# Performance work log

Hardware: AMD Instinct MI355X
Metric: run time of the kernel (lower is better)

The kernel has to match this reference:

```python
import jax, jax.numpy as jnp
import numpy as np

E = 128
H = 4
D = E // H  # 32


def setup_inputs() -> dict:
    key = jax.random.key(0)
    ks = jax.random.split(key, 5)
    b, n = 4, 4096
    x = jax.random.normal(ks[0], (b, n, E), dtype=jnp.float32)
    # Linear weights stored as [in, out] (i.e. torch weight transposed)
    W_qkv = jax.random.normal(ks[1], (E, 3 * E), dtype=jnp.float32) * (1.0 / np.sqrt(E))
    b_qkv = jax.random.normal(ks[2], (3 * E,), dtype=jnp.float32) * 0.01
    W_proj = jax.random.normal(ks[3], (E, E), dtype=jnp.float32) * (1.0 / np.sqrt(E))
    b_proj = jax.random.normal(ks[4], (E,), dtype=jnp.float32) * 0.01
    return {"x": x, "W_qkv": W_qkv, "b_qkv": b_qkv, "W_proj": W_proj, "b_proj": b_proj}


def reference(x, W_qkv, b_qkv, W_proj, b_proj):
    b, n, e = x.shape
    # qkv projection; last dim layout is (h d qkv) with qkv innermost,
    # matching rearrange('b n (h d qkv) -> qkv b h n d')
    qkv = (x @ W_qkv + b_qkv).reshape(b, n, H, D, 3)
    qkv = jnp.transpose(qkv, (4, 0, 2, 1, 3))  # [3, b, h, n, d]
    q, k, v = qkv[0], qkv[1], qkv[2]
    # NOTE: original scales by sqrt(e) (=sqrt(128)), not sqrt(d). Faithful.
    scale = 1.0 / np.float32(np.sqrt(e))
    scores = jnp.einsum('bhnd,bhmd->bhnm', q, k) * scale  # [b,h,n,n]
    att = jax.nn.softmax(scores, axis=-1)
    # dropout is identity in eval mode (reference baseline)
    out = jnp.einsum('bhnm,bhmd->bhnd', att, v)  # [b,h,n,d]
    out = jnp.transpose(out, (0, 2, 1, 3)).reshape(b, n, e)  # b n (h d)
    return out @ W_proj + b_proj
```

## Files before the change

### kernel.cpp

```cpp
#include <hip/hip_runtime.h>
#include <stdint.h>

#define N_SEQ 4096
#define MFMA16 __builtin_amdgcn_mfma_f32_16x16x32_bf16

typedef float f32x4 __attribute__((ext_vector_type(4)));
typedef float f32x2 __attribute__((ext_vector_type(2)));
typedef unsigned short u16x8 __attribute__((ext_vector_type(8)));
typedef unsigned short u16x4 __attribute__((ext_vector_type(4)));
typedef unsigned int u32x2 __attribute__((ext_vector_type(2)));
typedef __bf16 bf16x8 __attribute__((ext_vector_type(8)));

static __device__ __forceinline__ float bf2f(unsigned short u) {
    unsigned v = ((unsigned)u) << 16;
    return __builtin_bit_cast(float, v);
}

__global__ __launch_bounds__(256) void wrepack_kernel(
    const float* __restrict__ Wq, unsigned short* __restrict__ WqF)
{
    int idx = blockIdx.x * 256 + threadIdx.x;
    int i = idx & 7, l = (idx >> 3) & 63, fr = idx >> 9;
    int ct = fr >> 2, ks = fr & 3;
    int k = ks * 32 + (l >> 4) * 8 + i;
    int col = ct * 16 + (l & 15);
    WqF[idx] = __builtin_bit_cast(unsigned short, (__bf16)Wq[k * 384 + col]);
}

__global__ __launch_bounds__(256) void qkv_kernel(
    const float* __restrict__ x, const unsigned short* __restrict__ WqF,
    const float* __restrict__ bq, unsigned short* __restrict__ Qo,
    unsigned short* __restrict__ KFo, unsigned short* __restrict__ VFo)
{
    const int tid = threadIdx.x, lane = tid & 63, w = tid >> 6;
    const int g = lane >> 4, lo = lane & 15;
    const long r0 = (long)blockIdx.x * 32;
    const float SL = (float)(0.08838834764831845 * 1.4426950408889634);
    const f32x4 zf = {0.f, 0.f, 0.f, 0.f};

    bf16x8 xf[2][4];
    #pragma unroll
    for (int rt = 0; rt < 2; ++rt) {
        const float* xr = x + (r0 + rt * 16 + lo) * 128 + g * 8;
        #pragma unroll
        for (int ks = 0; ks < 4; ++ks) {
            f32x4 a = *(const f32x4*)&xr[ks * 32];
            f32x4 b = *(const f32x4*)&xr[ks * 32 + 4];
            bf16x8 f;
            f[0] = (__bf16)a[0]; f[1] = (__bf16)a[1]; f[2] = (__bf16)a[2]; f[3] = (__bf16)a[3];
            f[4] = (__bf16)b[0]; f[5] = (__bf16)b[1]; f[6] = (__bf16)b[2]; f[7] = (__bf16)b[3];
            xf[rt][ks] = f;
        }
    }
    f32x4 acc[2][6];
    #pragma unroll
    for (int rt = 0; rt < 2; ++rt)
        #pragma unroll
        for (int c = 0; c < 6; ++c) acc[rt][c] = zf;

    const u16x8* wp = (const u16x8*)WqF + (size_t)(w * 24) * 64 + lane;
    #pragma unroll
    for (int c = 0; c < 6; ++c)
        #pragma unroll
        for (int ks = 0; ks < 4; ++ks) {
            bf16x8 wf = __builtin_bit_cast(bf16x8, wp[(c * 4 + ks) * 64]);
            acc[0][c] = MFMA16(xf[0][ks], wf, acc[0][c], 0, 0, 0);
            acc[1][c] = MFMA16(xf[1][ks], wf, acc[1][c], 0, 0, 0);
        }

    const int bb = (int)(r0 >> 12), nn0 = (int)(r0 & 4095);
    const int bh = bb * 4 + w;
    const int t = nn0 >> 6, kvb = nn0 & 63;
    const int kk = kvb >> 5;
    #pragma unroll
    for (int c = 0; c < 6; ++c) {
        int col = (w * 6 + c) * 16 + lo;
        int rem = col - w * 96;
        int d = rem / 3, s = rem % 3;
        float bias = bq[col];
        #pragma unroll
        for (int rt = 0; rt < 2; ++rt) {
            float scale = (s == 0) ? SL : 1.0f;
            unsigned short bits[4];
            #pragma unroll
            for (int j = 0; j < 4; ++j)
                bits[j] = __builtin_bit_cast(unsigned short,
                              (__bf16)((acc[rt][c][j] + bias) * scale));
            if (s == 0) {
                long base = ((long)bh * 4096 + nn0 + rt * 16 + 4 * g) * 32 + d;
                #pragma unroll
                for (int j = 0; j < 4; ++j) Qo[base + (long)j * 32] = bits[j];
            } else if (s == 1) {
                int ct_k = (kvb >> 4) + rt;
                long base = (long)((bh * 64 + t) * 4 + ct_k) * 512
                          + ((d >> 3) * 16 + 4 * g) * 8 + (d & 7);
                #pragma unroll
                for (int j = 0; j < 4; ++j) KFo[base + j * 8] = bits[j];
            } else {
                int lg = rt * 2 + (g >> 1);
                long base = (long)(((bh * 64 + t) * 2 + kk) * 2 + (d >> 4)) * 512
                          + (lg * 16 + (d & 15)) * 8 + ((4 * g) & 7);
                u16x4 pk = {bits[0], bits[1], bits[2], bits[3]};
                *(u16x4*)&VFo[base] = pk;
            }
        }
    }
}

__global__ __launch_bounds__(256, 4) void attn_kernel(
    const unsigned short* __restrict__ Q, const unsigned short* __restrict__ KF,
    const unsigned short* __restrict__ VF, unsigned short* __restrict__ AO)
{
    __shared__ __align__(16) unsigned short P_lds[4][2][2048];

    const int tid = threadIdx.x, lane = tid & 63, w = tid >> 6;
    const int g = lane >> 4, lo = lane & 15;
    const int wq = w & 1, wh = w >> 1;

    const int bid = blockIdx.x;
    const int vid = (bid & 7) * 128 + (bid >> 3);
    const int qi = vid & 63, bh = vid >> 6;
    const int q0 = qi * 64 + wq * 32;

    bf16x8 qf[2];
    #pragma unroll
    for (int rt = 0; rt < 2; ++rt) {
        const unsigned short* p = Q + ((long)bh * 4096 + q0 + rt * 16 + lo) * 32 + g * 8;
        qf[rt] = __builtin_bit_cast(bf16x8, *(const u16x8*)p);
    }
    bf16x8 onesf;
    {
        u16x8 ou = {0x3F80,0x3F80,0x3F80,0x3F80,0x3F80,0x3F80,0x3F80,0x3F80};
        onesf = __builtin_bit_cast(bf16x8, ou);
    }
    const f32x4 zf = {0.f, 0.f, 0.f, 0.f};
    f32x4 o_[2][2] = {{zf, zf}, {zf, zf}};
    f32x4 ls[2]    = {zf, zf};

    int woff[2][4], roff[2][2];
    #pragma unroll
    for (int qt = 0; qt < 2; ++qt) {
        int q = lo + 16 * qt;
        #pragma unroll
        for (int ct = 0; ct < 4; ++ct) {
            int kvb = 16 * ct + 4 * g;
            woff[qt][ct] = q * 64 + (((kvb >> 3) ^ (q & 7)) * 8) + ((kvb >> 2) & 1) * 4;
        }
    }
    #pragma unroll
    for (int rt = 0; rt < 2; ++rt) {
        int q = lo + 16 * rt;
        #pragma unroll
        for (int kk = 0; kk < 2; ++kk)
            roff[rt][kk] = q * 64 + ((((4 * kk) + g) ^ (q & 7)) * 8);
    }
    unsigned short* B0 = &P_lds[w][0][0];
    unsigned short* B1 = &P_lds[w][1][0];

    const u16x8* kp = (const u16x8*)KF + ((long)bh * 64 + wh * 32) * 256 + lane;
    const u16x8* vp = (const u16x8*)VF + ((long)bh * 64 + wh * 32) * 256 + lane;

    u16x8 K0[4], K1[4], V0[4], V1[4];
    #pragma unroll
    for (int i = 0; i < 4; ++i) K0[i] = kp[i * 64];
    kp += 256;

#define BODY(KC, KN, VP, VC, BW, BR, DOPV) do {                                \
    _Pragma("unroll")                                                          \
    for (int i = 0; i < 4; ++i) KN[i] = kp[i * 64];                            \
    kp += 256;                                                                 \
    _Pragma("unroll")                                                          \
    for (int i = 0; i < 4; ++i) VC[i] = vp[i * 64];                            \
    vp += 256;                                                                 \
    u16x8 pa_[2][2];                                                           \
    if (DOPV) {                                                                \
        _Pragma("unroll")                                                      \
        for (int kk = 0; kk < 2; ++kk)                                         \
            _Pragma("unroll")                                                  \
            for (int rt = 0; rt < 2; ++rt)                                     \
                pa_[kk][rt] = *(const u16x8*)&BR[roff[rt][kk]];                \
    }                                                                          \
    f32x4 s_[2][4];                                                            \
    _Pragma("unroll")                                                          \
    for (int ct = 0; ct < 4; ++ct) {                                           \
        bf16x8 kfr = __builtin_bit_cast(bf16x8, KC[ct]);                       \
        s_[0][ct] = MFMA16(kfr, qf[0], zf, 0, 0, 0);                           \
        s_[1][ct] = MFMA16(kfr, qf[1], zf, 0, 0, 0);                           \
    }                                                                          \
    if (DOPV) {                                                                \
        _Pragma("unroll")                                                      \
        for (int kk = 0; kk < 2; ++kk)                                         \
            _Pragma("unroll")                                                  \
            for (int rt = 0; rt < 2; ++rt) {                                   \
                bf16x8 paf = __builtin_bit_cast(bf16x8, pa_[kk][rt]);          \
                ls[rt] = MFMA16(paf, onesf, ls[rt], 0, 0, 0);                  \
                o_[rt][0] = MFMA16(paf, __builtin_bit_cast(bf16x8, VP[kk*2+0]),\
                                   o_[rt][0], 0, 0, 0);                        \
                o_[rt][1] = MFMA16(paf, __builtin_bit_cast(bf16x8, VP[kk*2+1]),\
                                   o_[rt][1], 0, 0, 0);                        \
            }                                                                  \
    }                                                                          \
    _Pragma("unroll")                                                          \
    for (int qt = 0; qt < 2; ++qt)                                             \
        _Pragma("unroll")                                                      \
        for (int ct = 0; ct < 4; ++ct) {                                       \
            unsigned b0 = __builtin_bit_cast(unsigned,                         \
                __builtin_amdgcn_exp2f(s_[qt][ct][0])) + 0x8000u;              \
            unsigned b1 = __builtin_bit_cast(unsigned,                         \
                __builtin_amdgcn_exp2f(s_[qt][ct][1])) + 0x8000u;              \
            unsigned b2 = __builtin_bit_cast(unsigned,                         \
                __builtin_amdgcn_exp2f(s_[qt][ct][2])) + 0x8000u;              \
            unsigned b3 = __builtin_bit_cast(unsigned,                         \
                __builtin_amdgcn_exp2f(s_[qt][ct][3])) + 0x8000u;              \
            u32x2 wv_;                                                         \
            wv_[0] = __builtin_amdgcn_perm(b1, b0, 0x07060302u);               \
            wv_[1] = __builtin_amdgcn_perm(b3, b2, 0x07060302u);               \
            *(u16x4*)&BW[woff[qt][ct]] = __builtin_bit_cast(u16x4, wv_);       \
        }                                                                      \
    __builtin_amdgcn_sched_barrier(0);                                         \
} while (0)

    BODY(K0, K1, V1, V0, B0, B1, 0);
    #pragma unroll 1
    for (int t = 1; t < 31; t += 2) {
        BODY(K1, K0, V0, V1, B1, B0, 1);
        BODY(K0, K1, V1, V0, B0, B1, 1);
    }
    BODY(K1, K0, V0, V1, B1, B0, 1);
#undef BODY

    #pragma unroll
    for (int kk = 0; kk < 2; ++kk)
        #pragma unroll
        for (int rt = 0; rt < 2; ++rt) {
            bf16x8 paf = __builtin_bit_cast(bf16x8, *(const u16x8*)&B1[roff[rt][kk]]);
            ls[rt] = MFMA16(paf, onesf, ls[rt], 0, 0, 0);
            o_[rt][0] = MFMA16(paf, __builtin_bit_cast(bf16x8, V1[kk*2+0]), o_[rt][0], 0, 0, 0);
            o_[rt][1] = MFMA16(paf, __builtin_bit_cast(bf16x8, V1[kk*2+1]), o_[rt][1], 0, 0, 0);
        }

    __syncthreads();
    float* sc = (float*)&P_lds[0][0][0];
    float* myp = sc + (wq * 64 + lane) * 24;
    if (wh == 1) {
        #pragma unroll
        for (int rt = 0; rt < 2; ++rt)
            #pragma unroll
            for (int dt = 0; dt < 2; ++dt)
                *(f32x4*)&myp[(rt * 2 + dt) * 4] = o_[rt][dt];
        *(f32x4*)&myp[16] = ls[0];
        *(f32x4*)&myp[20] = ls[1];
    }
    __syncthreads();
    if (wh == 0) {
        #pragma unroll
        for (int rt = 0; rt < 2; ++rt) {
            #pragma unroll
            for (int dt = 0; dt < 2; ++dt)
                o_[rt][dt] += *(const f32x4*)&myp[(rt * 2 + dt) * 4];
            ls[rt] += *(const f32x4*)&myp[16 + rt * 4];
        }
        const int bb = bh >> 2, h = bh & 3;
        #pragma unroll
        for (int rt = 0; rt < 2; ++rt)
            #pragma unroll
            for (int j = 0; j < 4; ++j) {
                float rl = __builtin_amdgcn_rcpf(ls[rt][j]);
                int row = q0 + rt * 16 + 4 * g + j;
                #pragma unroll
                for (int dt = 0; dt < 2; ++dt) {
                    int e = h * 32 + lo + 16 * dt;
                    float val = o_[rt][dt][j] * rl;
                    AO[((long)bb * N_SEQ + row) * 128 + e] =
                        __builtin_bit_cast(unsigned short, (__bf16)val);
                }
            }
    }
}

__global__ __launch_bounds__(256) void proj_kernel(
    const unsigned short* __restrict__ ain, const float* __restrict__ Wp,
    const float* __restrict__ bp, float* __restrict__ out)
{
    __shared__ __align__(16) float xT[128][36];
    const int tid = threadIdx.x;
    const long r0 = (long)blockIdx.x * 32;
    #pragma unroll
    for (int i = 0; i < 2; ++i) {
        int idx = i * 256 + tid;
        int row = idx >> 4, kc = (idx & 15) * 8;
        u16x8 v = *(const u16x8*)&ain[(r0 + row) * 128 + kc];
        #pragma unroll
        for (int e = 0; e < 8; ++e) xT[kc + e][row] = bf2f(v[e]);
    }
    __syncthreads();
    const int r8 = (tid >> 6) * 8;
    const int c  = tid & 63;
    float acc0[8], acc1[8];
    #pragma unroll
    for (int r = 0; r < 8; ++r) { acc0[r] = 0.f; acc1[r] = 0.f; }
    for (int k = 0; k < 128; ++k) {
        f32x4 a0 = *(const f32x4*)&xT[k][r8];
        f32x4 a1 = *(const f32x4*)&xT[k][r8 + 4];
        float xr[8] = {a0[0],a0[1],a0[2],a0[3],a1[0],a1[1],a1[2],a1[3]};
        float w0 = Wp[k * 128 + c];
        float w1 = Wp[k * 128 + c + 64];
        #pragma unroll
        for (int r = 0; r < 8; ++r) {
            acc0[r] = fmaf(xr[r], w0, acc0[r]);
            acc1[r] = fmaf(xr[r], w1, acc1[r]);
        }
    }
    float b0 = bp[c], b1 = bp[c + 64];
    #pragma unroll
    for (int r = 0; r < 8; ++r) {
        long n = r0 + r8 + r;
        out[n * 128 + c]      = acc0[r] + b0;
        out[n * 128 + c + 64] = acc1[r] + b1;
    }
}

extern "C" void kernel_launch(void* const* d_in, const int* in_sizes, int n_in,
                              void* d_out, int out_size, void* d_ws, size_t ws_size,
                              hipStream_t stream)
{
    const float* x  = (const float*)d_in[0];
    const float* Wq = (const float*)d_in[1];
    const float* bq = (const float*)d_in[2];
    const float* Wp = (const float*)d_in[3];
    const float* bp = (const float*)d_in[4];
    float* out = (float*)d_out;

    unsigned short* Qw   = (unsigned short*)d_ws;
    unsigned short* KFw  = Qw  + (size_t)16 * 4096 * 32;
    unsigned short* VFw  = KFw + (size_t)16 * 4096 * 32;
    unsigned short* AOw  = VFw + (size_t)16 * 4096 * 32;
    unsigned short* WqFw = AOw + (size_t)16 * 4096 * 32;

    wrepack_kernel<<<192, 256, 0, stream>>>(Wq, WqFw);
    qkv_kernel<<<512, 256, 0, stream>>>(x, WqFw, bq, Qw, KFw, VFw);
    attn_kernel<<<1024, 256, 0, stream>>>(Qw, KFw, VFw, AOw);
    proj_kernel<<<512, 256, 0, stream>>>(AOw, Wp, bp, out);
}
```

Measured before the change: 93.22 us.

## Split attention KV range four ways per block with 32-query blocks

The attention kernel now gives each block 32 query rows and splits the KV sequence across all four waves, each taking a quarter. Before, each block held 64 queries split over two query waves and two KV halves. The grid doubles to 2048 blocks and the per-wave P staging drops from two LDS buffers to one, freeing shared memory for a three-way partial-sum combine with a padded stride of 25 floats. This aims at more parallelism and shorter per-wave loops. In exchange, each K/V tile is read for half as many queries, the cross-wave reduction is larger, and the odd stride makes the 16-byte LDS accesses unaligned.

```diff
diff --git a/kernel.cpp b/kernel.cpp
--- a/kernel.cpp
+++ b/kernel.cpp
@@ -111,16 +111,15 @@
     const unsigned short* __restrict__ Q, const unsigned short* __restrict__ KF,
     const unsigned short* __restrict__ VF, unsigned short* __restrict__ AO)
 {
-    __shared__ __align__(16) unsigned short P_lds[4][2][2048];
+    __shared__ __align__(16) unsigned char smem[19456];
 
     const int tid = threadIdx.x, lane = tid & 63, w = tid >> 6;
     const int g = lane >> 4, lo = lane & 15;
-    const int wq = w & 1, wh = w >> 1;
 
     const int bid = blockIdx.x;
-    const int vid = (bid & 7) * 128 + (bid >> 3);
-    const int qi = vid & 63, bh = vid >> 6;
-    const int q0 = qi * 64 + wq * 32;
+    const int vid = (bid & 7) * 256 + (bid >> 3);
+    const int qi = vid & 127, bh = vid >> 7;
+    const int q0 = qi * 32;
 
     bf16x8 qf[2];
     #pragma unroll
@@ -154,18 +153,17 @@
         for (int kk = 0; kk < 2; ++kk)
             roff[rt][kk] = q * 64 + ((((4 * kk) + g) ^ (q & 7)) * 8);
     }
-    unsigned short* B0 = &P_lds[w][0][0];
-    unsigned short* B1 = &P_lds[w][1][0];
-
-    const u16x8* kp = (const u16x8*)KF + ((long)bh * 64 + wh * 32) * 256 + lane;
-    const u16x8* vp = (const u16x8*)VF + ((long)bh * 64 + wh * 32) * 256 + lane;
+    unsigned short* B = (unsigned short*)(smem + w * 4096);
+
+    const u16x8* kp = (const u16x8*)KF + ((long)bh * 64 + w * 16) * 256 + lane;
+    const u16x8* vp = (const u16x8*)VF + ((long)bh * 64 + w * 16) * 256 + lane;
 
     u16x8 K0[4], K1[4], V0[4], V1[4];
     #pragma unroll
     for (int i = 0; i < 4; ++i) K0[i] = kp[i * 64];
     kp += 256;
 
-#define BODY(KC, KN, VP, VC, BW, BR, DOPV) do {                                \
+#define BODY(KC, KN, VP, VC, DOPV) do {                                        \
     _Pragma("unroll")                                                          \
     for (int i = 0; i < 4; ++i) KN[i] = kp[i * 64];                            \
     kp += 256;                                                                 \
@@ -178,7 +176,7 @@
         for (int kk = 0; kk < 2; ++kk)                                         \
             _Pragma("unroll")                                                  \
             for (int rt = 0; rt < 2; ++rt)                                     \
-                pa_[kk][rt] = *(const u16x8*)&BR[roff[rt][kk]];                \
+                pa_[kk][rt] = *(const u16x8*)&B[roff[rt][kk]];                 \
     }                                                                          \
     f32x4 s_[2][4];                                                            \
     _Pragma("unroll")                                                          \
@@ -215,34 +213,34 @@
             u32x2 wv_;                                                         \
             wv_[0] = __builtin_amdgcn_perm(b1, b0, 0x07060302u);               \
             wv_[1] = __builtin_amdgcn_perm(b3, b2, 0x07060302u);               \
-            *(u16x4*)&BW[woff[qt][ct]] = __builtin_bit_cast(u16x4, wv_);       \
+            *(u16x4*)&B[woff[qt][ct]] = __builtin_bit_cast(u16x4, wv_);        \
         }                                                                      \
     __builtin_amdgcn_sched_barrier(0);                                         \
 } while (0)
 
-    BODY(K0, K1, V1, V0, B0, B1, 0);
+    BODY(K0, K1, V1, V0, 0);
     #pragma unroll 1
-    for (int t = 1; t < 31; t += 2) {
-        BODY(K1, K0, V0, V1, B1, B0, 1);
-        BODY(K0, K1, V1, V0, B0, B1, 1);
-    }
-    BODY(K1, K0, V0, V1, B1, B0, 1);
+    for (int t = 1; t < 15; t += 2) {
+        BODY(K1, K0, V0, V1, 1);
+        BODY(K0, K1, V1, V0, 1);
+    }
+    BODY(K1, K0, V0, V1, 1);
 #undef BODY
 
     #pragma unroll
     for (int kk = 0; kk < 2; ++kk)
         #pragma unroll
         for (int rt = 0; rt < 2; ++rt) {
-            bf16x8 paf = __builtin_bit_cast(bf16x8, *(const u16x8*)&B1[roff[rt][kk]]);
+            bf16x8 paf = __builtin_bit_cast(bf16x8, *(const u16x8*)&B[roff[rt][kk]]);
             ls[rt] = MFMA16(paf, onesf, ls[rt], 0, 0, 0);
             o_[rt][0] = MFMA16(paf, __builtin_bit_cast(bf16x8, V1[kk*2+0]), o_[rt][0], 0, 0, 0);
             o_[rt][1] = MFMA16(paf, __builtin_bit_cast(bf16x8, V1[kk*2+1]), o_[rt][1], 0, 0, 0);
         }
 
     __syncthreads();
-    float* sc = (float*)&P_lds[0][0][0];
-    float* myp = sc + (wq * 64 + lane) * 24;
-    if (wh == 1) {
+    float* comb = (float*)smem;
+    if (w > 0) {
+        float* myp = comb + ((w - 1) * 64 + lane) * 25;
         #pragma unroll
         for (int rt = 0; rt < 2; ++rt)
             #pragma unroll
@@ -252,13 +250,17 @@
         *(f32x4*)&myp[20] = ls[1];
     }
     __syncthreads();
-    if (wh == 0) {
-        #pragma unroll
-        for (int rt = 0; rt < 2; ++rt) {
+    if (w == 0) {
+        #pragma unroll
+        for (int i = 0; i < 3; ++i) {
+            const float* pp = comb + (i * 64 + lane) * 25;
             #pragma unroll
-            for (int dt = 0; dt < 2; ++dt)
-                o_[rt][dt] += *(const f32x4*)&myp[(rt * 2 + dt) * 4];
-            ls[rt] += *(const f32x4*)&myp[16 + rt * 4];
+            for (int rt = 0; rt < 2; ++rt) {
+                #pragma unroll
+                for (int dt = 0; dt < 2; ++dt)
+                    o_[rt][dt] += *(const f32x4*)&pp[(rt * 2 + dt) * 4];
+                ls[rt] += *(const f32x4*)&pp[16 + rt * 4];
+            }
         }
         const int bb = bh >> 2, h = bh & 3;
         #pragma unroll
@@ -339,6 +341,6 @@
 
     wrepack_kernel<<<192, 256, 0, stream>>>(Wq, WqFw);
     qkv_kernel<<<512, 256, 0, stream>>>(x, WqFw, bq, Qw, KFw, VFw);
-    attn_kernel<<<1024, 256, 0, stream>>>(Qw, KFw, VFw, AOw);
+    attn_kernel<<<2048, 256, 0, stream>>>(Qw, KFw, VFw, AOw);
     proj_kernel<<<512, 256, 0, stream>>>(AOw, Wp, bp, out);
 }
```

New measurement: 95.70 us. 1.03x slower.
